# Kernel tuning notes

Measured on AMD Instinct MI355X. Metric: run time of the kernel, lower is better.

## Reference

```python
import jax, jax.numpy as jnp
import numpy as np

H = W = 256          # input_img_height (square images)
N_NODES = 8          # camera graph nodes
N_EDGES = 64         # ~fully connected directed graph
FEAT = 1024          # edge_feat_dim
BN_EPS = 1e-5


def setup_inputs() -> dict:
    key = jax.random.key(0)
    ks = jax.random.split(key, 8)
    d = {}
    d["x"] = jax.random.normal(ks[0], (N_NODES, 3 * H * W), dtype=jnp.float32)
    d["edge_index"] = jax.random.randint(ks[1], (2, N_EDGES), 0, N_NODES)
    # ResNet stem params (conv1 replaced to take 6 channels)
    d["conv1_w"] = jax.random.normal(ks[2], (64, 6, 7, 7), dtype=jnp.float32) * 0.05
    d["bn_gamma"] = jnp.ones((64,), jnp.float32)
    d["bn_beta"] = jnp.zeros((64,), jnp.float32)
    d["bn_mean"] = jnp.zeros((64,), jnp.float32)
    d["bn_var"] = jnp.ones((64,), jnp.float32)
    d["fc_w"] = jax.random.normal(ks[3], (FEAT, 64), dtype=jnp.float32) * 0.05
    d["fc_b"] = jnp.zeros((FEAT,), jnp.float32)
    d["fc_xyz_w"] = jax.random.normal(ks[4], (3, FEAT), dtype=jnp.float32) * 0.05
    d["fc_xyz_b"] = jnp.zeros((3,), jnp.float32)
    d["fc_wpqr_w"] = jax.random.normal(ks[5], (3, FEAT), dtype=jnp.float32) * 0.05
    d["fc_wpqr_b"] = jnp.zeros((3,), jnp.float32)
    return d


def _edge_extractor(ef, conv1_w, bn_gamma, bn_beta, bn_mean, bn_var, fc_w, fc_b):
    # conv1: 6->64, 7x7, stride 2, pad 3, no bias
    y = jax.lax.conv_general_dilated(
        ef, conv1_w, window_strides=(2, 2), padding=[(3, 3), (3, 3)],
        dimension_numbers=("NCHW", "OIHW", "NCHW"))
    # BatchNorm (inference form with running stats), fused scale/shift
    scale = (bn_gamma * jax.lax.rsqrt(bn_var + BN_EPS))[None, :, None, None]
    shift = (bn_beta - bn_mean * bn_gamma * jax.lax.rsqrt(bn_var + BN_EPS))[None, :, None, None]
    y = jax.nn.relu(y * scale + shift)
    # maxpool 3x3 stride 2 pad 1
    y = jax.lax.reduce_window(y, -jnp.inf, jax.lax.max,
                              (1, 1, 3, 3), (1, 1, 2, 2),
                              [(0, 0), (0, 0), (1, 1), (1, 1)])
    # AdaptiveAvgPool2d(1) + fc to edge_feat_dim
    y = jnp.mean(y, axis=(2, 3))                     # [E, 64]
    return y @ fc_w.T + fc_b                         # [E, FEAT]


def reference(x, edge_index, conv1_w, bn_gamma, bn_beta, bn_mean, bn_var,
              fc_w, fc_b, fc_xyz_w, fc_xyz_b, fc_wpqr_w, fc_wpqr_b):
    imgs = x.reshape(N_NODES, 3, H, W)
    # compute_edge_features, vectorized: gather min/max node per edge, concat channels
    nmin = jnp.min(edge_index, axis=0)               # [E]
    nmax = jnp.max(edge_index, axis=0)               # [E]
    edge_feat = jnp.concatenate([imgs[nmin], imgs[nmax]], axis=1)  # [E, 6, H, W]
    ef = _edge_extractor(edge_feat, conv1_w, bn_gamma, bn_beta, bn_mean, bn_var, fc_w, fc_b)
    ef = jax.nn.relu(ef)
    # droprate == 0 -> no dropout
    xyz = ef @ fc_xyz_w.T + fc_xyz_b                 # [E, 3]
    wpqr = ef @ fc_wpqr_w.T + fc_wpqr_b              # [E, 3]
    full = jnp.concatenate([xyz, wpqr], axis=1)      # [E, 6]
    return (full[:N_NODES], full)
```

## Files before the change

kernel.cpp:

```cpp
#include <hip/hip_runtime.h>
#include <hip/hip_bf16.h>

#define N_NODES 8
#define N_EDGES 64
#define CO 64
#define OH 128
#define OW 128
#define FEAT 1024
#define BN_EPS 1e-5f

#define OFF_PARTIAL 0
#define OFF_WB      3471616
#define OFF_A       3520768
#define OFF_B       20297984
#define OFF_FCWT    37075200

#define RS_W 136

typedef short bf16x8 __attribute__((ext_vector_type(8)));
typedef float f32x4  __attribute__((ext_vector_type(4)));

__device__ __forceinline__ unsigned short f2bf(float f) {
    unsigned u = __float_as_uint(f);
    u += 0x7fffu + ((u >> 16) & 1u);
    return (unsigned short)(u >> 16);
}
__device__ __forceinline__ float blo(unsigned u) { return __uint_as_float(u << 16); }
__device__ __forceinline__ float bhi(unsigned u) { return __uint_as_float(u & 0xffff0000u); }

__global__ __launch_bounds__(256) void prep_kernel(
        const float* __restrict__ w,
        const float* __restrict__ gamma, const float* __restrict__ var,
        const float* __restrict__ fc_w,
        unsigned short* __restrict__ wb2, float* __restrict__ fc_wT) {
    int idx = blockIdx.x * 256 + threadIdx.x;
    if (idx < 2 * 64 * 192) {
        int tp = idx % 192;
        int c  = (idx / 192) & 63;
        int h  = idx / (192 * 64);
        int rr = tp >> 3, kx = tp & 7;
        float val = 0.f;
        if (rr < 21 && kx >= 1) {
            int ci = rr / 7, ky = rr % 7;
            float sc = gamma[c] * rsqrtf(var[c] + BN_EPS);
            val = w[((c * 6 + h * 3 + ci) * 7 + ky) * 7 + (kx - 1)] * sc;
        }
        wb2[(rr * 128 + h * 64 + c) * 8 + kx] = f2bf(val);
    }
    if (idx < CO * FEAT) {
        int c = idx >> 10, f = idx & 1023;
        fc_wT[idx] = fc_w[f * CO + c];
    }
}

__global__ __launch_bounds__(256, 3) void conv_kernel(
        const float* __restrict__ x, const unsigned short* __restrict__ wb2,
        const float* __restrict__ gamma, const float* __restrict__ beta,
        const float* __restrict__ mean,  const float* __restrict__ var,
        unsigned short* __restrict__ A2, unsigned short* __restrict__ B2) {
    int bx  = blockIdx.x;
    int r16 = bx & 7;
    int idx = bx >> 3;
    int n   = idx >> 4;
    int oy  = (r16 << 4) + (idx & 15);
    int t   = threadIdx.x;

    __shared__ __align__(16) char smem[32768];
    unsigned* rawu = (unsigned*)smem;

    if (t < 168) {
        int rr = t >> 3, wsel = t & 7;
        int u = (wsel < 2) ? wsel : (128 + wsel);
        rawu[rr * RS_W + u] = 0u;
    } else if (t < 270) {
        int k2 = t - 168;
        int rr = 21 + k2 / 34, g = k2 % 34;
        *(uint4*)&rawu[rr * RS_W + 4 * g] = make_uint4(0u, 0u, 0u, 0u);
    }

    const float* xn = x + (size_t)n * (3 * 65536);
    for (int k = t; k < 1344; k += 256) {
        int rr = k >> 6, q = k & 63;
        int ci = (rr * 147) >> 10;
        int ky = rr - ci * 7;
        int iy = 2 * oy + ky - 3;
        uint2 pk = make_uint2(0u, 0u);
        if ((unsigned)iy < 256u) {
            float4 f = *(const float4*)(xn + ci * 65536 + iy * 256 + 4 * q);
            pk.x = (unsigned)f2bf(f.x) | ((unsigned)f2bf(f.y) << 16);
            pk.y = (unsigned)f2bf(f.z) | ((unsigned)f2bf(f.w) << 16);
        }
        *(uint2*)&rawu[rr * RS_W + 2 * q + 2] = pk;
    }
    __syncthreads();

    int wv = t >> 6, lane = t & 63;
    int hg = wv >> 1;
    int wg = wv & 1;
    int quad = lane >> 4, m = lane & 15;

    f32x4 acc[4][4];
#pragma unroll
    for (int ct = 0; ct < 4; ++ct)
#pragma unroll
        for (int nt = 0; nt < 4; ++nt)
            acc[ct][nt] = (f32x4){0.f, 0.f, 0.f, 0.f};

    const bf16x8* wbv = (const bf16x8*)wb2;

#pragma unroll 2
    for (int s = 0; s < 6; ++s) {
        int rq = 4 * s + quad;
        bf16x8 afrag[4];
#pragma unroll
        for (int nt = 0; nt < 4; ++nt) {
            int ox = 64 * wg + 16 * nt + m;
            int base = rq * RS_W + ox;
            union { unsigned u[4]; bf16x8 v; } bb;
            bb.u[0] = rawu[base];     bb.u[1] = rawu[base + 1];
            bb.u[2] = rawu[base + 2]; bb.u[3] = rawu[base + 3];
            afrag[nt] = bb.v;
        }
#pragma unroll
        for (int ct = 0; ct < 4; ++ct) {
            bf16x8 wfrag = wbv[rq * 128 + hg * 64 + 16 * ct + m];
#pragma unroll
            for (int nt = 0; nt < 4; ++nt)
                acc[ct][nt] = __builtin_amdgcn_mfma_f32_16x16x32_bf16(
                                  afrag[nt], wfrag, acc[ct][nt], 0, 0, 0);
        }
    }

    float sh[4] = {0.f, 0.f, 0.f, 0.f};
    if (hg) {
#pragma unroll
        for (int ct = 0; ct < 4; ++ct) {
            int c = 16 * ct + m;
            float sc = gamma[c] * rsqrtf(var[c] + BN_EPS);
            sh[ct] = beta[c] - mean[c] * sc;
        }
    }

    __syncthreads();
    unsigned short* T = (unsigned short*)smem;

#pragma unroll
    for (int ct = 0; ct < 4; ++ct) {
        int chp = hg * 64 + 16 * ct + m;
        int sw  = (chp & 7) << 2;
#pragma unroll
        for (int nt = 0; nt < 4; ++nt) {
            int px0 = 64 * wg + 16 * nt + 4 * quad;
            float v0 = acc[ct][nt][0] + sh[ct];
            float v1 = acc[ct][nt][1] + sh[ct];
            float v2 = acc[ct][nt][2] + sh[ct];
            float v3 = acc[ct][nt][3] + sh[ct];
            uint2 pk;
            pk.x = (unsigned)f2bf(v0) | ((unsigned)f2bf(v1) << 16);
            pk.y = (unsigned)f2bf(v2) | ((unsigned)f2bf(v3) << 16);
            int gs = ((px0 >> 2) ^ sw);
            *(uint2*)&T[chp * 128 + gs * 4] = pk;
        }
    }
    __syncthreads();

#pragma unroll
    for (int rr = 0; rr < 4; ++rr) {
        int row = rr * 32 + (t >> 3), slot = t & 7;
        int hh = row >> 6, ch = row & 63;
        int swr = (row & 7) << 2;
        unsigned short* dst = (hh ? B2 : A2)
                            + ((size_t)(n * CO + ch) << 14) + (oy << 7) + slot * 16;
#pragma unroll
        for (int i = 0; i < 2; ++i) {
            int g  = slot * 4 + i * 2;
            int gs = g ^ swr;
            *(uint4*)(dst + i * 8) = *(uint4*)&T[row * 128 + gs * 4];
        }
    }
}

__global__ __launch_bounds__(256, 4) void pool_kernel(
        const unsigned short* __restrict__ A2,
        const unsigned short* __restrict__ B2,
        float* __restrict__ partial) {
    int pb  = blockIdx.x;
    int xcd = pb & 7;
    int q   = pb >> 3;
    int c   = q >> 1;
    int rt  = xcd * 2 + (q & 1);
    int t   = threadIdx.x;

    __shared__ unsigned short S[2 * 8 * 9 * 128];

    for (int k = t; k < 2304; k += 256) {
        int slot = k & 15;
        int r    = (k >> 4) % 9;
        int tn   = (k >> 4) / 9;
        int grow = 8 * rt - 1 + r;
        uint4 v = make_uint4(0u, 0u, 0u, 0u);
        if (grow >= 0) {
            const unsigned short* src = (tn >= 8) ? B2 : A2;
            int node = tn & 7;
            v = *(const uint4*)(src + ((size_t)(node * CO + c) << 14)
                                    + (grow << 7) + slot * 8);
        }
        *(uint4*)&S[tn * 1152 + (r << 7) + slot * 8] = v;
    }
    __syncthreads();

    int wv = t >> 6, lane = t & 63;
    int esub = lane >> 4, tc = lane & 15;

    for (int i = 0; i < 3; ++i) {
        int sidx = 12 * wv + 4 * i + esub;
        bool valid = sidx < 36;
        int ss = valid ? sidx : 0;
        int pi = 0, rem = ss;
        while (rem >= 8 - pi) { rem -= 8 - pi; ++pi; }
        int pj = pi + rem;
        const unsigned short* pa  = &S[pi * 1152];
        const unsigned short* pb2 = &S[(8 + pj) * 1152];

        float mx[4][4];
#pragma unroll
        for (int p = 0; p < 4; ++p)
#pragma unroll
            for (int qq = 0; qq < 4; ++qq) mx[p][qq] = 0.f;

#pragma unroll
        for (int r = 0; r < 9; ++r) {
            uint4 ga = *(const uint4*)(pa + (r << 7) + tc * 8);
            uint4 gb = *(const uint4*)(pb2 + (r << 7) + tc * 8);
            float ha = 0.f, hb = 0.f;
            if (tc > 0) {
                ha = bhi(*(const unsigned*)(pa + (r << 7) + tc * 8 - 2));
                hb = bhi(*(const unsigned*)(pb2 + (r << 7) + tc * 8 - 2));
            }
            float z0 = ha + hb;
            float z1 = blo(ga.x) + blo(gb.x), z2 = bhi(ga.x) + bhi(gb.x);
            float z3 = blo(ga.y) + blo(gb.y), z4 = bhi(ga.y) + bhi(gb.y);
            float z5 = blo(ga.z) + blo(gb.z), z6 = bhi(ga.z) + bhi(gb.z);
            float z7 = blo(ga.w) + blo(gb.w), z8 = bhi(ga.w) + bhi(gb.w);
            float h0 = fmaxf(fmaxf(z0, z1), z2);
            float h1 = fmaxf(fmaxf(z2, z3), z4);
            float h2 = fmaxf(fmaxf(z4, z5), z6);
            float h3 = fmaxf(fmaxf(z6, z7), z8);
            if (r & 1) {
                int p = (r - 1) >> 1;
                mx[p][0] = fmaxf(mx[p][0], h0); mx[p][1] = fmaxf(mx[p][1], h1);
                mx[p][2] = fmaxf(mx[p][2], h2); mx[p][3] = fmaxf(mx[p][3], h3);
            } else {
                if (r >= 2) {
                    int p = (r >> 1) - 1;
                    mx[p][0] = fmaxf(mx[p][0], h0); mx[p][1] = fmaxf(mx[p][1], h1);
                    mx[p][2] = fmaxf(mx[p][2], h2); mx[p][3] = fmaxf(mx[p][3], h3);
                }
                if (r <= 6) {
                    int p = r >> 1;
                    mx[p][0] = fmaxf(mx[p][0], h0); mx[p][1] = fmaxf(mx[p][1], h1);
                    mx[p][2] = fmaxf(mx[p][2], h2); mx[p][3] = fmaxf(mx[p][3], h3);
                }
            }
        }

        float sum = 0.f;
#pragma unroll
        for (int p = 0; p < 4; ++p)
#pragma unroll
            for (int qq = 0; qq < 4; ++qq) sum += fmaxf(mx[p][qq], 0.f);

        sum += __shfl_down(sum, 8, 64);
        sum += __shfl_down(sum, 4, 64);
        sum += __shfl_down(sum, 2, 64);
        sum += __shfl_down(sum, 1, 64);
        if (tc == 0 && valid)
            partial[(rt * 36 + sidx) * 64 + c] = sum;
    }
}

__global__ __launch_bounds__(1024) void head_kernel(
        const int* __restrict__ ei, const float* __restrict__ partial,
        const float* __restrict__ fc_wT,  const float* __restrict__ fc_b,
        const float* __restrict__ xyz_w,  const float* __restrict__ xyz_b,
        const float* __restrict__ wpqr_w, const float* __restrict__ wpqr_b,
        float* __restrict__ out) {
    int e = blockIdx.x;
    int t = threadIdx.x;
    int a0 = ei[e], a1 = ei[N_EDGES + e];
    int pi = min(a0, a1), pj = max(a0, a1);
    int rank = pi * 8 - ((pi * (pi + 1)) >> 1) + pj;
    __shared__ float pl[CO];
    if (t < CO) {
        float s = 0.f;
#pragma unroll
        for (int rt = 0; rt < 16; ++rt)
            s += partial[(rt * 36 + rank) * 64 + t];
        pl[t] = s * (1.f / 4096.f);
    }
    __syncthreads();

    float d = fc_b[t];
#pragma unroll
    for (int c = 0; c < CO; ++c)
        d = fmaf(pl[c], fc_wT[c * FEAT + t], d);
    d = fmaxf(d, 0.f);

    float s[6];
#pragma unroll
    for (int r = 0; r < 3; ++r) {
        s[r]     = d * xyz_w[r * FEAT + t];
        s[3 + r] = d * wpqr_w[r * FEAT + t];
    }
#pragma unroll
    for (int r = 0; r < 6; ++r)
#pragma unroll
        for (int off = 32; off > 0; off >>= 1)
            s[r] += __shfl_down(s[r], off, 64);

    __shared__ float red[16][6];
    if ((t & 63) == 0) {
#pragma unroll
        for (int r = 0; r < 6; ++r) red[t >> 6][r] = s[r];
    }
    __syncthreads();
    if (t < 6) {
        float v = 0.f;
#pragma unroll
        for (int w = 0; w < 16; ++w) v += red[w][t];
        v += (t < 3) ? xyz_b[t] : wpqr_b[t - 3];
        out[48 + e * 6 + t] = v;
        if (e < 8) out[e * 6 + t] = v;
    }
}

extern "C" void kernel_launch(void* const* d_in, const int* in_sizes, int n_in,
                              void* d_out, int out_size, void* d_ws, size_t ws_size,
                              hipStream_t stream) {
    const float* x        = (const float*)d_in[0];
    const int*   ei       = (const int*)d_in[1];
    const float* conv1_w  = (const float*)d_in[2];
    const float* bn_gamma = (const float*)d_in[3];
    const float* bn_beta  = (const float*)d_in[4];
    const float* bn_mean  = (const float*)d_in[5];
    const float* bn_var   = (const float*)d_in[6];
    const float* fc_w     = (const float*)d_in[7];
    const float* fc_b     = (const float*)d_in[8];
    const float* xyz_w    = (const float*)d_in[9];
    const float* xyz_b    = (const float*)d_in[10];
    const float* wpqr_w   = (const float*)d_in[11];
    const float* wpqr_b   = (const float*)d_in[12];
    float* out = (float*)d_out;

    char* ws = (char*)d_ws;
    float*          partial = (float*)(ws + OFF_PARTIAL);
    unsigned short* wb2     = (unsigned short*)(ws + OFF_WB);
    unsigned short* A2      = (unsigned short*)(ws + OFF_A);
    unsigned short* B2      = (unsigned short*)(ws + OFF_B);
    float*          fc_wT   = (float*)(ws + OFF_FCWT);

    prep_kernel<<<256, 256, 0, stream>>>(conv1_w, bn_gamma, bn_var,
                                         fc_w, wb2, fc_wT);
    conv_kernel<<<1024, 256, 0, stream>>>(x, wb2, bn_gamma, bn_beta,
                                          bn_mean, bn_var, A2, B2);
    pool_kernel<<<1024, 256, 0, stream>>>(A2, B2, partial);
    head_kernel<<<64, 1024, 0, stream>>>(ei, partial, fc_wT, fc_b,
                                         xyz_w, xyz_b, wpqr_w, wpqr_b, out);
}
```

Measured before the change: 119.3 us.

## Fuse head into pool kernel using a global completion counter

```diff
diff --git a/kernel.cpp b/kernel.cpp
--- a/kernel.cpp
+++ b/kernel.cpp
@@ -10,6 +10,7 @@
 #define BN_EPS 1e-5f
 
 #define OFF_PARTIAL 0
+#define OFF_DONE    151552
 #define OFF_WB      3471616
 #define OFF_A       3520768
 #define OFF_B       20297984
@@ -32,8 +33,11 @@
         const float* __restrict__ w,
         const float* __restrict__ gamma, const float* __restrict__ var,
         const float* __restrict__ fc_w,
-        unsigned short* __restrict__ wb2, float* __restrict__ fc_wT) {
+        unsigned short* __restrict__ wb2, float* __restrict__ fc_wT,
+        unsigned* __restrict__ done) {
     int idx = blockIdx.x * 256 + threadIdx.x;
+    if (idx == 0)
+        __hip_atomic_store(done, 0u, __ATOMIC_RELAXED, __HIP_MEMORY_SCOPE_AGENT);
     if (idx < 2 * 64 * 192) {
         int tp = idx % 192;
         int c  = (idx / 192) & 63;
@@ -180,10 +184,15 @@
     }
 }
 
-__global__ __launch_bounds__(256, 4) void pool_kernel(
+__global__ __launch_bounds__(256, 4) void pool_head_kernel(
         const unsigned short* __restrict__ A2,
         const unsigned short* __restrict__ B2,
-        float* __restrict__ partial) {
+        float* __restrict__ partial, unsigned* __restrict__ done,
+        const int* __restrict__ ei,
+        const float* __restrict__ fc_wT,  const float* __restrict__ fc_b,
+        const float* __restrict__ xyz_w,  const float* __restrict__ xyz_b,
+        const float* __restrict__ wpqr_w, const float* __restrict__ wpqr_b,
+        float* __restrict__ out) {
     int pb  = blockIdx.x;
     int xcd = pb & 7;
     int q   = pb >> 3;
@@ -277,57 +286,71 @@
         if (tc == 0 && valid)
             partial[(rt * 36 + sidx) * 64 + c] = sum;
     }
-}
-
-__global__ __launch_bounds__(1024) void head_kernel(
-        const int* __restrict__ ei, const float* __restrict__ partial,
-        const float* __restrict__ fc_wT,  const float* __restrict__ fc_b,
-        const float* __restrict__ xyz_w,  const float* __restrict__ xyz_b,
-        const float* __restrict__ wpqr_w, const float* __restrict__ wpqr_b,
-        float* __restrict__ out) {
-    int e = blockIdx.x;
-    int t = threadIdx.x;
+
+    __syncthreads();
+    if (t == 0) {
+        __threadfence();
+        __hip_atomic_fetch_add(done, 1u, __ATOMIC_RELEASE,
+                               __HIP_MEMORY_SCOPE_AGENT);
+    }
+    if (pb >= N_EDGES) return;
+
+    int e = pb;
     int a0 = ei[e], a1 = ei[N_EDGES + e];
-    int pi = min(a0, a1), pj = max(a0, a1);
-    int rank = pi * 8 - ((pi * (pi + 1)) >> 1) + pj;
-    __shared__ float pl[CO];
+    int ppi = min(a0, a1), ppj = max(a0, a1);
+    int rank = ppi * 8 - ((ppi * (ppi + 1)) >> 1) + ppj;
+    float fb[4];
+#pragma unroll
+    for (int ff = 0; ff < 4; ++ff) fb[ff] = fc_b[ff * 256 + t];
+
+    if (t == 0) {
+        while (__hip_atomic_load(done, __ATOMIC_ACQUIRE,
+                                 __HIP_MEMORY_SCOPE_AGENT) < 1024u)
+            __builtin_amdgcn_s_sleep(1);
+        __threadfence();
+    }
+    __syncthreads();
+
+    float* pl  = (float*)S;
+    float* red = pl + 64;
     if (t < CO) {
         float s = 0.f;
 #pragma unroll
-        for (int rt = 0; rt < 16; ++rt)
-            s += partial[(rt * 36 + rank) * 64 + t];
+        for (int rr = 0; rr < 16; ++rr)
+            s += partial[(rr * 36 + rank) * 64 + t];
         pl[t] = s * (1.f / 4096.f);
     }
     __syncthreads();
 
-    float d = fc_b[t];
-#pragma unroll
-    for (int c = 0; c < CO; ++c)
-        d = fmaf(pl[c], fc_wT[c * FEAT + t], d);
-    d = fmaxf(d, 0.f);
-
-    float s[6];
-#pragma unroll
-    for (int r = 0; r < 3; ++r) {
-        s[r]     = d * xyz_w[r * FEAT + t];
-        s[3 + r] = d * wpqr_w[r * FEAT + t];
+    float s6[6] = {0.f, 0.f, 0.f, 0.f, 0.f, 0.f};
+#pragma unroll
+    for (int ff = 0; ff < 4; ++ff) {
+        int f = ff * 256 + t;
+        float d = fb[ff];
+#pragma unroll
+        for (int cc = 0; cc < CO; ++cc)
+            d = fmaf(pl[cc], fc_wT[cc * FEAT + f], d);
+        d = fmaxf(d, 0.f);
+#pragma unroll
+        for (int r = 0; r < 3; ++r) {
+            s6[r]     = fmaf(d, xyz_w[r * FEAT + f],  s6[r]);
+            s6[3 + r] = fmaf(d, wpqr_w[r * FEAT + f], s6[3 + r]);
+        }
     }
 #pragma unroll
     for (int r = 0; r < 6; ++r)
 #pragma unroll
         for (int off = 32; off > 0; off >>= 1)
-            s[r] += __shfl_down(s[r], off, 64);
-
-    __shared__ float red[16][6];
+            s6[r] += __shfl_down(s6[r], off, 64);
+
     if ((t & 63) == 0) {
 #pragma unroll
-        for (int r = 0; r < 6; ++r) red[t >> 6][r] = s[r];
+        for (int r = 0; r < 6; ++r) red[(t >> 6) * 6 + r] = s6[r];
     }
     __syncthreads();
     if (t < 6) {
-        float v = 0.f;
-#pragma unroll
-        for (int w = 0; w < 16; ++w) v += red[w][t];
+        float v = red[0 * 6 + t] + red[1 * 6 + t]
+                + red[2 * 6 + t] + red[3 * 6 + t];
         v += (t < 3) ? xyz_b[t] : wpqr_b[t - 3];
         out[48 + e * 6 + t] = v;
         if (e < 8) out[e * 6 + t] = v;
@@ -354,16 +377,17 @@
 
     char* ws = (char*)d_ws;
     float*          partial = (float*)(ws + OFF_PARTIAL);
+    unsigned*       done    = (unsigned*)(ws + OFF_DONE);
     unsigned short* wb2     = (unsigned short*)(ws + OFF_WB);
     unsigned short* A2      = (unsigned short*)(ws + OFF_A);
     unsigned short* B2      = (unsigned short*)(ws + OFF_B);
     float*          fc_wT   = (float*)(ws + OFF_FCWT);
 
     prep_kernel<<<256, 256, 0, stream>>>(conv1_w, bn_gamma, bn_var,
-                                         fc_w, wb2, fc_wT);
+                                         fc_w, wb2, fc_wT, done);
     conv_kernel<<<1024, 256, 0, stream>>>(x, wb2, bn_gamma, bn_beta,
                                           bn_mean, bn_var, A2, B2);
-    pool_kernel<<<1024, 256, 0, stream>>>(A2, B2, partial);
-    head_kernel<<<64, 1024, 0, stream>>>(ei, partial, fc_wT, fc_b,
-                                         xyz_w, xyz_b, wpqr_w, wpqr_b, out);
-}
+    pool_head_kernel<<<1024, 256, 0, stream>>>(A2, B2, partial, done, ei,
+                                               fc_wT, fc_b, xyz_w, xyz_b,
+                                               wpqr_w, wpqr_b, out);
+}
```

Result: slower. 189.6 us (+58.9%).
